# Optimization experiments

Measured on AMD Instinct MI355X. Metric: run time of the kernel, lower is better.

## Reference

```python
import jax, jax.numpy as jnp
import numpy as np

B, S, HID = 4, 2048, 1024
NH, HD = 16, 64  # op_heads, head_size (hidden_size // total_heads)
EPS = 1e-6


def setup_inputs() -> dict:
    key = jax.random.key(0)
    k1, k2, k3, k4 = jax.random.split(key, 4)
    return {
        "hidden_states": jax.random.normal(k1, (B, S, HID), dtype=jnp.float32),
        "assoc_hc_attn": jax.random.uniform(k2, (B, S, S), dtype=jnp.float32),
        "broad_hc_attn": jax.random.uniform(k3, (B, S, S), dtype=jnp.float32),
        "Wv": jax.random.normal(k4, (HID, NH * HD), dtype=jnp.float32) * 0.02,
        "bv": jnp.zeros((NH * HD,), dtype=jnp.float32),
    }


def reference(hidden_states, assoc_hc_attn, broad_hc_attn, Wv, bv):
    # v_proj + split heads -> [B, NH, S, HD]
    value = hidden_states @ Wv + bv
    sp_value = value.reshape(B, S, NH, HD).transpose(0, 2, 1, 3)

    # broad_heads == 0, so attn_heads == assoc_hc_attn broadcast over all op_heads.
    attn = assoc_hc_attn.astype(jnp.float32)  # [B, S, S]
    causal = jnp.tril(jnp.ones((S, S), dtype=bool))
    attn = jnp.where(causal, attn, 0.0)
    # sum-normalize along keys (no softmax)
    attn = attn / (EPS + attn.sum(axis=-1, keepdims=True))

    # shared attn across heads: contract once -> [B, NH, S, HD]
    out = jnp.einsum('bqk,bhkd->bhqd', attn, sp_value)
    # merge heads -> [B, S, NH*HD]
    return out.transpose(0, 2, 1, 3).reshape(B, S, NH * HD)
```

## Files before the change

kernel.cpp:

```cpp
#include <hip/hip_runtime.h>

#define B_    4
#define S_    2048
#define HID_  1024
#define NO_   1024
#define EPS_  1e-6f
#define M1_   (B_ * S_)

typedef __attribute__((ext_vector_type(8))) short  short8;
typedef __attribute__((ext_vector_type(4))) float  f32x4;
typedef unsigned short ushort_t;

__device__ __forceinline__ unsigned short f2bf(float f) {
  union { float f; unsigned int u; } v; v.f = f;
  unsigned int r = v.u + 0x7FFFu + ((v.u >> 16) & 1u);
  return (unsigned short)(r >> 16);
}
__device__ __forceinline__ unsigned pack2(float a, float b) {
  return (unsigned)f2bf(a) | ((unsigned)f2bf(b) << 16);
}

typedef __attribute__((address_space(1))) const void GASV;
typedef __attribute__((address_space(3))) void LASV;
__device__ __forceinline__ void gld16(const void* g, void* l) {
  __builtin_amdgcn_global_load_lds((GASV*)g, (LASV*)l, 16, 0, 0);
}

__global__ void k_twv(const float* __restrict__ Wv, ushort_t* __restrict__ WvT) {
  __shared__ float tile[32][33];
  int k0 = blockIdx.x * 32;
  int n0 = blockIdx.y * 32;
  int tx = threadIdx.x, ty = threadIdx.y;
  for (int i = ty; i < 32; i += 8)
    tile[i][tx] = Wv[(size_t)(k0 + i) * NO_ + n0 + tx];
  __syncthreads();
  for (int i = ty; i < 32; i += 8)
    WvT[(size_t)(n0 + i) * HID_ + k0 + tx] = f2bf(tile[tx][i]);
}

__global__ __launch_bounds__(256) void k_cvtH(const float* __restrict__ H,
                                              ushort_t* __restrict__ Hb) {
  size_t i = ((size_t)blockIdx.x * 256 + threadIdx.x) * 4;
  float4 v = *(const float4*)(H + i);
  uint2 p; p.x = pack2(v.x, v.y); p.y = pack2(v.z, v.w);
  *(uint2*)(Hb + i) = p;
}

__global__ __launch_bounds__(256) void k_prepA(const float* __restrict__ A,
                                               ushort_t* __restrict__ Ab) {
  int row  = blockIdx.x * 4 + (threadIdx.x >> 6);
  int lane = threadIdx.x & 63;
  int q = row & 2047;
  int wend = ((q >> 7) + 1) << 7;
  const float* rp = A + (size_t)row * S_;
  float4 v[8];
  float s = 0.f;
#pragma unroll
  for (int i = 0; i < 8; i++) {
    int k = i * 256 + lane * 4;
    if (k < wend) {
      float4 t = *(const float4*)(rp + k);
      t.x = (k + 0 <= q) ? t.x : 0.f;
      t.y = (k + 1 <= q) ? t.y : 0.f;
      t.z = (k + 2 <= q) ? t.z : 0.f;
      t.w = (k + 3 <= q) ? t.w : 0.f;
      v[i] = t;
      s += t.x + t.y + t.z + t.w;
    }
  }
  for (int off = 1; off < 64; off <<= 1) s += __shfl_xor(s, off, 64);
  float inv = 1.0f / (EPS_ + s);
  ushort_t* op = Ab + (size_t)row * S_;
#pragma unroll
  for (int i = 0; i < 8; i++) {
    int k = i * 256 + lane * 4;
    if (k < wend) {
      uint2 p;
      p.x = pack2(v[i].x * inv, v[i].y * inv);
      p.y = pack2(v[i].z * inv, v[i].w * inv);
      *(uint2*)(op + k) = p;
    }
  }
}

__global__ __launch_bounds__(128) void k_vt(
    const ushort_t* __restrict__ WvT, const ushort_t* __restrict__ Hb,
    const float* __restrict__ bv, ushort_t* __restrict__ Vt) {
  __shared__ __align__(16) ushort_t lds_a[64 * 32];
  __shared__ __align__(16) ushort_t lds_b[128 * 32];
  int m0 = blockIdx.x * 128;
  int n0 = blockIdx.y * 64;
  int tid = threadIdx.x;
  int wave = tid >> 6, lane = tid & 63;
  int lq = lane >> 4, lm = lane & 15;

  int rr = lane >> 2;
  int sc = (lane & 3) ^ ((rr >> 1) & 3);
  const ushort_t* gA = WvT + (size_t)(n0 + wave * 32 + rr) * HID_ + sc * 8;
  const ushort_t* gB = Hb  + (size_t)(m0 + wave * 64 + rr) * HID_ + sc * 8;
  char* la = (char*)lds_a;
  char* lb = (char*)lds_b;
  char* la_w = la + wave * 2048;
  char* lb_w = lb + wave * 4096;
  int swz = (lm >> 1) & 3;
  int fo = (lq ^ swz) << 4;

  f32x4 acc[4][4];
  for (int i = 0; i < 4; i++) for (int j = 0; j < 4; j++) acc[i][j] = (f32x4)0.0f;

  for (int it = 0; it < HID_ / 32; it++) {
    gld16(gA,               la_w);
    gld16(gA + 16 * HID_,   la_w + 1024);
    gld16(gB,               lb_w);
    gld16(gB + 16 * HID_,   lb_w + 1024);
    gld16(gB + 32 * HID_,   lb_w + 2048);
    gld16(gB + 48 * HID_,   lb_w + 3072);
    gA += 32; gB += 32;
    __syncthreads();
    short8 af[4], bfr[4];
#pragma unroll
    for (int mi = 0; mi < 4; mi++)
      af[mi] = *(const short8*)(la + (mi * 16 + lm) * 64 + fo);
#pragma unroll
    for (int ni = 0; ni < 4; ni++)
      bfr[ni] = *(const short8*)(lb + (wave * 64 + ni * 16 + lm) * 64 + fo);
#pragma unroll
    for (int mi = 0; mi < 4; mi++)
#pragma unroll
      for (int ni = 0; ni < 4; ni++)
        acc[mi][ni] = __builtin_amdgcn_mfma_f32_16x16x32_bf16(af[mi], bfr[ni], acc[mi][ni], 0, 0, 0);
    __syncthreads();
  }
  for (int mi = 0; mi < 4; mi++) {
    for (int r = 0; r < 4; r++) {
      int n = n0 + mi * 16 + lq * 4 + r;
      float bias = bv[n];
      for (int ni = 0; ni < 4; ni++) {
        int m = m0 + wave * 64 + ni * 16 + lm;
        int b = m >> 11;
        int s = m & 2047;
        Vt[((size_t)b * NO_ + n) * S_ + s] = f2bf(acc[mi][ni][r] + bias);
      }
    }
  }
}

__global__ __launch_bounds__(128) void k_attn(
    const ushort_t* __restrict__ Ab, const ushort_t* __restrict__ Vt,
    float* __restrict__ out) {
  __shared__ __align__(16) ushort_t lds_a[128 * 32];
  __shared__ __align__(16) ushort_t lds_b[64 * 32];
  int col = blockIdx.x;
  int n0 = (col & 15) * 64;
  int b  = col >> 4;
  int t  = 15 - (int)blockIdx.y;
  int q0 = t * 128;
  int tid = threadIdx.x;
  int wave = tid >> 6, lane = tid & 63;
  int lq = lane >> 4, lm = lane & 15;

  int rr = lane >> 2;
  int sc = (lane & 3) ^ ((rr >> 1) & 3);
  const ushort_t* gA = Ab + ((size_t)(b * S_ + q0 + wave * 64 + rr)) * S_ + sc * 8;
  const ushort_t* gB = Vt + ((size_t)(b * NO_ + n0 + wave * 32 + rr)) * S_ + sc * 8;
  char* la = (char*)lds_a;
  char* lb = (char*)lds_b;
  char* la_w = la + wave * 4096;
  char* lb_w = lb + wave * 2048;
  int swz = (lm >> 1) & 3;
  int fo = (lq ^ swz) << 4;

  f32x4 acc[4][4];
  for (int i = 0; i < 4; i++) for (int j = 0; j < 4; j++) acc[i][j] = (f32x4)0.0f;

  const int iters = (q0 >> 5) + 4;
  for (int it = 0; it < iters; it++) {
    gld16(gA,             la_w);
    gld16(gA + 16 * S_,   la_w + 1024);
    gld16(gA + 32 * S_,   la_w + 2048);
    gld16(gA + 48 * S_,   la_w + 3072);
    gld16(gB,             lb_w);
    gld16(gB + 16 * S_,   lb_w + 1024);
    gA += 32; gB += 32;
    __syncthreads();
    short8 af[4], bfr[4];
#pragma unroll
    for (int mi = 0; mi < 4; mi++)
      af[mi] = *(const short8*)(la + (wave * 64 + mi * 16 + lm) * 64 + fo);
#pragma unroll
    for (int ni = 0; ni < 4; ni++)
      bfr[ni] = *(const short8*)(lb + (ni * 16 + lm) * 64 + fo);
#pragma unroll
    for (int mi = 0; mi < 4; mi++)
#pragma unroll
      for (int ni = 0; ni < 4; ni++)
        acc[mi][ni] = __builtin_amdgcn_mfma_f32_16x16x32_bf16(af[mi], bfr[ni], acc[mi][ni], 0, 0, 0);
    __syncthreads();
  }
  for (int mi = 0; mi < 4; mi++) {
    for (int r = 0; r < 4; r++) {
      int q = q0 + wave * 64 + mi * 16 + lq * 4 + r;
      for (int ni = 0; ni < 4; ni++) {
        int n = n0 + ni * 16 + lm;
        out[((size_t)b * S_ + q) * NO_ + n] = acc[mi][ni][r];
      }
    }
  }
}

extern "C" void kernel_launch(void* const* d_in, const int* in_sizes, int n_in,
                              void* d_out, int out_size, void* d_ws, size_t ws_size,
                              hipStream_t stream) {
  const float* H  = (const float*)d_in[0];
  const float* A  = (const float*)d_in[1];
  const float* Wv = (const float*)d_in[3];
  const float* bv = (const float*)d_in[4];
  float* out = (float*)d_out;

  char* ws = (char*)d_ws;
  ushort_t* WvT = (ushort_t*)ws;
  ushort_t* Hb  = (ushort_t*)(ws + 2097152);
  ushort_t* Vt  = (ushort_t*)(ws + 2097152 + 16777216);
  ushort_t* Abf = (ushort_t*)(ws + 2097152 + 2 * 16777216);

  k_twv  <<<dim3(HID_ / 32, NO_ / 32), dim3(32, 8), 0, stream>>>(Wv, WvT);
  k_cvtH <<<(M1_ * HID_) / (256 * 4), 256, 0, stream>>>(H, Hb);
  k_prepA<<<M1_ / 4, 256, 0, stream>>>(A, Abf);
  k_vt   <<<dim3(M1_ / 128, NO_ / 64), 128, 0, stream>>>(WvT, Hb, bv, Vt);
  k_attn <<<dim3(64, 16), 128, 0, stream>>>(Abf, Vt, out);
}
```

Measured before the change: 246.1 us.

## Merge prep kernels and enlarge GEMM tiles to 128x128 with four waves

Folds the three conversion/normalization kernels into one launch that dispatches on block index, removing two kernel launches. Both MFMA GEMMs move from 128x64 tiles on two waves to 128x128 tiles on four waves arranged 2x2, so each loaded tile is reused across more output and global traffic per FLOP drops. The attention grid interleaves heavy and light causal row tiles to balance load. The cost is half as many blocks (512 for attention), which may leave fewer workgroups per CU to hide latency.

```diff
diff --git a/kernel.cpp b/kernel.cpp
--- a/kernel.cpp
+++ b/kernel.cpp
@@ -26,82 +26,83 @@
   __builtin_amdgcn_global_load_lds((GASV*)g, (LASV*)l, 16, 0, 0);
 }
 
-__global__ void k_twv(const float* __restrict__ Wv, ushort_t* __restrict__ WvT) {
-  __shared__ float tile[32][33];
-  int k0 = blockIdx.x * 32;
-  int n0 = blockIdx.y * 32;
-  int tx = threadIdx.x, ty = threadIdx.y;
-  for (int i = ty; i < 32; i += 8)
-    tile[i][tx] = Wv[(size_t)(k0 + i) * NO_ + n0 + tx];
-  __syncthreads();
-  for (int i = ty; i < 32; i += 8)
-    WvT[(size_t)(n0 + i) * HID_ + k0 + tx] = f2bf(tile[tx][i]);
-}
-
-__global__ __launch_bounds__(256) void k_cvtH(const float* __restrict__ H,
-                                              ushort_t* __restrict__ Hb) {
-  size_t i = ((size_t)blockIdx.x * 256 + threadIdx.x) * 4;
-  float4 v = *(const float4*)(H + i);
-  uint2 p; p.x = pack2(v.x, v.y); p.y = pack2(v.z, v.w);
-  *(uint2*)(Hb + i) = p;
-}
-
-__global__ __launch_bounds__(256) void k_prepA(const float* __restrict__ A,
-                                               ushort_t* __restrict__ Ab) {
-  int row  = blockIdx.x * 4 + (threadIdx.x >> 6);
-  int lane = threadIdx.x & 63;
-  int q = row & 2047;
-  int wend = ((q >> 7) + 1) << 7;
-  const float* rp = A + (size_t)row * S_;
-  float4 v[8];
-  float s = 0.f;
-#pragma unroll
-  for (int i = 0; i < 8; i++) {
-    int k = i * 256 + lane * 4;
-    if (k < wend) {
-      float4 t = *(const float4*)(rp + k);
-      t.x = (k + 0 <= q) ? t.x : 0.f;
-      t.y = (k + 1 <= q) ? t.y : 0.f;
-      t.z = (k + 2 <= q) ? t.z : 0.f;
-      t.w = (k + 3 <= q) ? t.w : 0.f;
-      v[i] = t;
-      s += t.x + t.y + t.z + t.w;
-    }
-  }
-  for (int off = 1; off < 64; off <<= 1) s += __shfl_xor(s, off, 64);
-  float inv = 1.0f / (EPS_ + s);
-  ushort_t* op = Ab + (size_t)row * S_;
-#pragma unroll
-  for (int i = 0; i < 8; i++) {
-    int k = i * 256 + lane * 4;
-    if (k < wend) {
-      uint2 p;
-      p.x = pack2(v[i].x * inv, v[i].y * inv);
-      p.y = pack2(v[i].z * inv, v[i].w * inv);
-      *(uint2*)(op + k) = p;
-    }
-  }
-}
-
-__global__ __launch_bounds__(128) void k_vt(
+__global__ __launch_bounds__(256) void k_prep(
+    const float* __restrict__ Wv, ushort_t* __restrict__ WvT,
+    const float* __restrict__ H,  ushort_t* __restrict__ Hb,
+    const float* __restrict__ A,  ushort_t* __restrict__ Ab) {
+  int id = blockIdx.x;
+  if (id < 1024) {
+    __shared__ float tile[32][33];
+    int k0 = (id & 31) * 32;
+    int n0 = (id >> 5) * 32;
+    int tx = threadIdx.x & 31, ty = threadIdx.x >> 5;
+    for (int i = ty; i < 32; i += 8)
+      tile[i][tx] = Wv[(size_t)(k0 + i) * NO_ + n0 + tx];
+    __syncthreads();
+    for (int i = ty; i < 32; i += 8)
+      WvT[(size_t)(n0 + i) * HID_ + k0 + tx] = f2bf(tile[tx][i]);
+  } else if (id < 1024 + 8192) {
+    size_t i = ((size_t)(id - 1024) * 256 + threadIdx.x) * 4;
+    float4 v = *(const float4*)(H + i);
+    uint2 p; p.x = pack2(v.x, v.y); p.y = pack2(v.z, v.w);
+    *(uint2*)(Hb + i) = p;
+  } else {
+    int row  = (id - 9216) * 4 + (threadIdx.x >> 6);
+    int lane = threadIdx.x & 63;
+    int q = row & 2047;
+    int wend = ((q >> 7) + 1) << 7;
+    const float* rp = A + (size_t)row * S_;
+    float4 v[8];
+    float s = 0.f;
+#pragma unroll
+    for (int i = 0; i < 8; i++) {
+      int k = i * 256 + lane * 4;
+      if (k < wend) {
+        float4 t = *(const float4*)(rp + k);
+        t.x = (k + 0 <= q) ? t.x : 0.f;
+        t.y = (k + 1 <= q) ? t.y : 0.f;
+        t.z = (k + 2 <= q) ? t.z : 0.f;
+        t.w = (k + 3 <= q) ? t.w : 0.f;
+        v[i] = t;
+        s += t.x + t.y + t.z + t.w;
+      }
+    }
+    for (int off = 1; off < 64; off <<= 1) s += __shfl_xor(s, off, 64);
+    float inv = 1.0f / (EPS_ + s);
+    ushort_t* op = Ab + (size_t)row * S_;
+#pragma unroll
+    for (int i = 0; i < 8; i++) {
+      int k = i * 256 + lane * 4;
+      if (k < wend) {
+        uint2 p;
+        p.x = pack2(v[i].x * inv, v[i].y * inv);
+        p.y = pack2(v[i].z * inv, v[i].w * inv);
+        *(uint2*)(op + k) = p;
+      }
+    }
+  }
+}
+
+__global__ __launch_bounds__(256) void k_vt(
     const ushort_t* __restrict__ WvT, const ushort_t* __restrict__ Hb,
     const float* __restrict__ bv, ushort_t* __restrict__ Vt) {
-  __shared__ __align__(16) ushort_t lds_a[64 * 32];
+  __shared__ __align__(16) ushort_t lds_a[128 * 32];
   __shared__ __align__(16) ushort_t lds_b[128 * 32];
   int m0 = blockIdx.x * 128;
-  int n0 = blockIdx.y * 64;
+  int n0 = blockIdx.y * 128;
   int tid = threadIdx.x;
   int wave = tid >> 6, lane = tid & 63;
   int lq = lane >> 4, lm = lane & 15;
+  int wr = wave >> 1, wc = wave & 1;
 
   int rr = lane >> 2;
   int sc = (lane & 3) ^ ((rr >> 1) & 3);
   const ushort_t* gA = WvT + (size_t)(n0 + wave * 32 + rr) * HID_ + sc * 8;
-  const ushort_t* gB = Hb  + (size_t)(m0 + wave * 64 + rr) * HID_ + sc * 8;
+  const ushort_t* gB = Hb  + (size_t)(m0 + wave * 32 + rr) * HID_ + sc * 8;
   char* la = (char*)lds_a;
   char* lb = (char*)lds_b;
   char* la_w = la + wave * 2048;
-  char* lb_w = lb + wave * 4096;
+  char* lb_w = lb + wave * 2048;
   int swz = (lm >> 1) & 3;
   int fo = (lq ^ swz) << 4;
 
@@ -113,17 +114,15 @@
     gld16(gA + 16 * HID_,   la_w + 1024);
     gld16(gB,               lb_w);
     gld16(gB + 16 * HID_,   lb_w + 1024);
-    gld16(gB + 32 * HID_,   lb_w + 2048);
-    gld16(gB + 48 * HID_,   lb_w + 3072);
     gA += 32; gB += 32;
     __syncthreads();
     short8 af[4], bfr[4];
 #pragma unroll
     for (int mi = 0; mi < 4; mi++)
-      af[mi] = *(const short8*)(la + (mi * 16 + lm) * 64 + fo);
+      af[mi] = *(const short8*)(la + (wr * 64 + mi * 16 + lm) * 64 + fo);
 #pragma unroll
     for (int ni = 0; ni < 4; ni++)
-      bfr[ni] = *(const short8*)(lb + (wave * 64 + ni * 16 + lm) * 64 + fo);
+      bfr[ni] = *(const short8*)(lb + (wc * 64 + ni * 16 + lm) * 64 + fo);
 #pragma unroll
     for (int mi = 0; mi < 4; mi++)
 #pragma unroll
@@ -133,10 +132,10 @@
   }
   for (int mi = 0; mi < 4; mi++) {
     for (int r = 0; r < 4; r++) {
-      int n = n0 + mi * 16 + lq * 4 + r;
+      int n = n0 + wr * 64 + mi * 16 + lq * 4 + r;
       float bias = bv[n];
       for (int ni = 0; ni < 4; ni++) {
-        int m = m0 + wave * 64 + ni * 16 + lm;
+        int m = m0 + wc * 64 + ni * 16 + lm;
         int b = m >> 11;
         int s = m & 2047;
         Vt[((size_t)b * NO_ + n) * S_ + s] = f2bf(acc[mi][ni][r] + bias);
@@ -145,27 +144,29 @@
   }
 }
 
-__global__ __launch_bounds__(128) void k_attn(
+__global__ __launch_bounds__(256) void k_attn(
     const ushort_t* __restrict__ Ab, const ushort_t* __restrict__ Vt,
     float* __restrict__ out) {
   __shared__ __align__(16) ushort_t lds_a[128 * 32];
-  __shared__ __align__(16) ushort_t lds_b[64 * 32];
+  __shared__ __align__(16) ushort_t lds_b[128 * 32];
   int col = blockIdx.x;
-  int n0 = (col & 15) * 64;
-  int b  = col >> 4;
-  int t  = 15 - (int)blockIdx.y;
+  int n0 = (col & 7) * 128;
+  int b  = col >> 3;
+  int y  = (int)blockIdx.y;
+  int t  = (y < 8) ? (15 - y) : (y - 8);
   int q0 = t * 128;
   int tid = threadIdx.x;
   int wave = tid >> 6, lane = tid & 63;
   int lq = lane >> 4, lm = lane & 15;
+  int wr = wave >> 1, wc = wave & 1;
 
   int rr = lane >> 2;
   int sc = (lane & 3) ^ ((rr >> 1) & 3);
-  const ushort_t* gA = Ab + ((size_t)(b * S_ + q0 + wave * 64 + rr)) * S_ + sc * 8;
+  const ushort_t* gA = Ab + ((size_t)(b * S_ + q0 + wave * 32 + rr)) * S_ + sc * 8;
   const ushort_t* gB = Vt + ((size_t)(b * NO_ + n0 + wave * 32 + rr)) * S_ + sc * 8;
   char* la = (char*)lds_a;
   char* lb = (char*)lds_b;
-  char* la_w = la + wave * 4096;
+  char* la_w = la + wave * 2048;
   char* lb_w = lb + wave * 2048;
   int swz = (lm >> 1) & 3;
   int fo = (lq ^ swz) << 4;
@@ -173,12 +174,10 @@
   f32x4 acc[4][4];
   for (int i = 0; i < 4; i++) for (int j = 0; j < 4; j++) acc[i][j] = (f32x4)0.0f;
 
-  const int iters = (q0 >> 5) + 4;
+  const int iters = 4 * t + 4;
   for (int it = 0; it < iters; it++) {
     gld16(gA,             la_w);
     gld16(gA + 16 * S_,   la_w + 1024);
-    gld16(gA + 32 * S_,   la_w + 2048);
-    gld16(gA + 48 * S_,   la_w + 3072);
     gld16(gB,             lb_w);
     gld16(gB + 16 * S_,   lb_w + 1024);
     gA += 32; gB += 32;
@@ -186,10 +185,10 @@
     short8 af[4], bfr[4];
 #pragma unroll
     for (int mi = 0; mi < 4; mi++)
-      af[mi] = *(const short8*)(la + (wave * 64 + mi * 16 + lm) * 64 + fo);
+      af[mi] = *(const short8*)(la + (wr * 64 + mi * 16 + lm) * 64 + fo);
 #pragma unroll
     for (int ni = 0; ni < 4; ni++)
-      bfr[ni] = *(const short8*)(lb + (ni * 16 + lm) * 64 + fo);
+      bfr[ni] = *(const short8*)(lb + (wc * 64 + ni * 16 + lm) * 64 + fo);
 #pragma unroll
     for (int mi = 0; mi < 4; mi++)
 #pragma unroll
@@ -199,10 +198,10 @@
   }
   for (int mi = 0; mi < 4; mi++) {
     for (int r = 0; r < 4; r++) {
-      int q = q0 + wave * 64 + mi * 16 + lq * 4 + r;
+      int q = q0 + wr * 64 + mi * 16 + lq * 4 + r;
       for (int ni = 0; ni < 4; ni++) {
-        int n = n0 + ni * 16 + lm;
-        out[((size_t)b * S_ + q) * NO_ + n] = acc[mi][ni][r];
+        int n = n0 + wc * 64 + ni * 16 + lm;
+        out[((size_t)(b * S_ + q)) * NO_ + n] = acc[mi][ni][r];
       }
     }
   }
@@ -223,9 +222,7 @@
   ushort_t* Vt  = (ushort_t*)(ws + 2097152 + 16777216);
   ushort_t* Abf = (ushort_t*)(ws + 2097152 + 2 * 16777216);
 
-  k_twv  <<<dim3(HID_ / 32, NO_ / 32), dim3(32, 8), 0, stream>>>(Wv, WvT);
-  k_cvtH <<<(M1_ * HID_) / (256 * 4), 256, 0, stream>>>(H, Hb);
-  k_prepA<<<M1_ / 4, 256, 0, stream>>>(A, Abf);
-  k_vt   <<<dim3(M1_ / 128, NO_ / 64), 128, 0, stream>>>(WvT, Hb, bv, Vt);
-  k_attn <<<dim3(64, 16), 128, 0, stream>>>(Abf, Vt, out);
-}
+  k_prep <<<1024 + 8192 + 2048, 256, 0, stream>>>(Wv, WvT, H, Hb, A, Abf);
+  k_vt   <<<dim3(M1_ / 128, NO_ / 128), 256, 0, stream>>>(WvT, Hb, bv, Vt);
+  k_attn <<<dim3(32, 16), 256, 0, stream>>>(Abf, Vt, out);
+}
```

Result: faster. 238.4 us (-3.1%).
